# Performance work log

Hardware: AMD Instinct MI355X
Metric: run time of the kernel (lower is better)

## Reference

```python
import jax, jax.numpy as jnp
import numpy as np

NUM_CLASSES = 1000
FEAT_DIM = 512
BATCH = 16384


def setup_inputs() -> dict:
    key = jax.random.key(0)
    k1, k2, k3 = jax.random.split(key, 3)
    x = jax.random.normal(k1, (BATCH, FEAT_DIM), dtype=jnp.float32)
    labels = jax.random.randint(k2, (BATCH,), 0, NUM_CLASSES, dtype=jnp.int64)
    centers = jax.random.normal(k3, (NUM_CLASSES, FEAT_DIM), dtype=jnp.float32)
    margin = jnp.ones((1,), dtype=jnp.float32)
    return {"x": x, "labels": labels, "centers": centers, "margin": margin}


def reference(x, labels, centers, margin):
    # squared euclidean distances: [B, C]
    distmat = (
        jnp.sum(x * x, axis=1, keepdims=True)
        + jnp.sum(centers * centers, axis=1)[None, :]
        - 2.0 * (x @ centers.T)
    )
    B, C = distmat.shape
    onehot = labels[:, None] == jnp.arange(C, dtype=labels.dtype)[None, :]  # [B, C]
    # distance to the true-class center
    dist = jnp.sum(jnp.where(onehot, distmat, 0.0), axis=1)  # [B]
    # min distance over all other classes (mask true class with +inf)
    dist_min = jnp.min(jnp.where(onehot, jnp.inf, distmat), axis=1)  # [B]
    m = margin[0]
    loss = jnp.sum(jnp.maximum(m + dist - dist_min, 0.0)) / B
    return loss
```

## Files before the change

kernel.cpp:

```cpp
#include <hip/hip_runtime.h>
#include <hip/hip_bf16.h>

#define BATCH 16384
#define NCLS  1000
#define NPAD  1024
#define FDIM  512

#define CBLK_STRIDE 266240
#define TAIL_OFF    262144

typedef __bf16 bf16x4 __attribute__((ext_vector_type(4)));
typedef __bf16 bf16x8 __attribute__((ext_vector_type(8)));
typedef float  f32x16 __attribute__((ext_vector_type(16)));

#define GLOBAL_AS __attribute__((address_space(1)))
#define LDS_AS    __attribute__((address_space(3)))

#define VMCNT(n) asm volatile("s_waitcnt vmcnt(" #n ")" ::: "memory")
#define LGKM0()  asm volatile("s_waitcnt lgkmcnt(0)" ::: "memory")
#define BAR()    do { LGKM0(); __builtin_amdgcn_s_barrier(); \
                      __builtin_amdgcn_sched_barrier(0); } while (0)

__global__ __launch_bounds__(64) void prep_centers(
    const float* __restrict__ centers, char* __restrict__ cbt,
    float* __restrict__ out)
{
    const int c = blockIdx.x, t = threadIdx.x;
    const int cblk = c >> 8, cl = c & 255;
    char* base = cbt + (size_t)cblk * CBLK_STRIDE;
    if (c == 0 && t == 0) out[0] = 0.f;

    float4 f0 = make_float4(0.f, 0.f, 0.f, 0.f);
    float4 f1 = make_float4(0.f, 0.f, 0.f, 0.f);
    if (c < NCLS) {
        f0 = *(const float4*)(centers + (size_t)c * FDIM + t * 8);
        f1 = *(const float4*)(centers + (size_t)c * FDIM + t * 8 + 4);
    }
    bf16x8 b;
    b[0] = (__bf16)f0.x; b[1] = (__bf16)f0.y; b[2] = (__bf16)f0.z; b[3] = (__bf16)f0.w;
    b[4] = (__bf16)f1.x; b[5] = (__bf16)f1.y; b[6] = (__bf16)f1.z; b[7] = (__bf16)f1.w;
    *(bf16x8*)(base + (t >> 2) * 16384 + (t & 3) * 4096 + cl * 16) = b;

    float ssum = f0.x*f0.x + f0.y*f0.y + f0.z*f0.z + f0.w*f0.w
               + f1.x*f1.x + f1.y*f1.y + f1.z*f1.z + f1.w*f1.w;
    #pragma unroll
    for (int o = 32; o > 0; o >>= 1) ssum += __shfl_down(ssum, o);
    if (t == 0) {
        const float hf = (c < NCLS) ? (-0.5f * ssum) : -1e30f;
        const __bf16 h = (__bf16)hf;
        const __bf16 l = (c < NCLS) ? (__bf16)(hf - (float)h) : (__bf16)0.f;
        bf16x8 tl;
        #pragma unroll
        for (int e = 0; e < 8; ++e) tl[e] = (__bf16)0.f;
        tl[0] = h; tl[1] = l;
        *(bf16x8*)(base + TAIL_OFF + cl * 16) = tl;
    }
}

struct B2 { float4 a, b; };

__global__ __launch_bounds__(512, 4) void trip_main(
    const float* __restrict__ x, const int* __restrict__ labels,
    const char* __restrict__ cbt, float* __restrict__ mxp,
    float* __restrict__ dap)
{
    extern __shared__ char lds[];
    const int t    = threadIdx.x;
    const int lane = t & 63;
    const int w    = t >> 6;
    const int wM   = w >> 1, wN = w & 1;
    const int l31  = lane & 31, hi = lane >> 5;
    const int bid  = blockIdx.x;
    const int cblk = bid >> 7;
    const int bblk = bid & 127;
    const int class0 = cblk * 256;
    const int row0   = bblk * 128;
    const char* cbB  = cbt + (size_t)cblk * CBLK_STRIDE;

    auto stageA = [&](int ko, int ai) {
        const char* src = cbB + ko * 16384 + t * 16;
        char* dst = lds + ai * 16384 + t * 16;
        __builtin_amdgcn_global_load_lds((const GLOBAL_AS void*)src,
                                         (LDS_AS void*)dst, 16, 0, 0);
        __builtin_amdgcn_global_load_lds((const GLOBAL_AS void*)(src + 8192),
                                         (LDS_AS void*)(dst + 8192), 16, 0, 0);
    };
    auto loadB = [&](int ko, B2& br) {
        const float* src = x + (size_t)(row0 + w * 16 + (lane >> 3)) * FDIM
                         + ko * 32 + (lane & 7) * 4;
        br.a = *(const float4*)(src);
        br.b = *(const float4*)(src + 8 * FDIM);
    };
    auto cv4 = [](float4 f) {
        bf16x4 v;
        v[0] = (__bf16)f.x; v[1] = (__bf16)f.y;
        v[2] = (__bf16)f.z; v[3] = (__bf16)f.w;
        return v;
    };
    auto writeB = [&](const B2& br, int bi) {
        char* dst = lds + 32768 + bi * 8192 + ((lane & 7) >> 1) * 2048
                  + (w * 16 + (lane >> 3)) * 16 + (lane & 1) * 8;
        *(bf16x4*)(dst      ) = cv4(br.a);
        *(bf16x4*)(dst + 128) = cv4(br.b);
    };

    f32x16 acc[2][2];
    #pragma unroll
    for (int mi = 0; mi < 2; ++mi)
        #pragma unroll
        for (int ni = 0; ni < 2; ++ni)
            #pragma unroll
            for (int r = 0; r < 16; ++r) acc[mi][ni][r] = 0.f;

    auto compute = [&](int buf) {
        const char* A = lds + buf * 16384;
        const char* B = lds + 32768 + buf * 8192;
        #pragma unroll
        for (int ks = 0; ks < 2; ++ks) {
            const int chunk = ks * 2 + hi;
            bf16x8 a0 = *(const bf16x8*)(A + chunk * 4096 + (wM * 64 +  0 + l31) * 16);
            bf16x8 a1 = *(const bf16x8*)(A + chunk * 4096 + (wM * 64 + 32 + l31) * 16);
            bf16x8 b0 = *(const bf16x8*)(B + chunk * 2048 + (wN * 64 +  0 + l31) * 16);
            bf16x8 b1 = *(const bf16x8*)(B + chunk * 2048 + (wN * 64 + 32 + l31) * 16);
            acc[0][0] = __builtin_amdgcn_mfma_f32_32x32x16_bf16(a0, b0, acc[0][0], 0, 0, 0);
            acc[0][1] = __builtin_amdgcn_mfma_f32_32x32x16_bf16(a0, b1, acc[0][1], 0, 0, 0);
            acc[1][0] = __builtin_amdgcn_mfma_f32_32x32x16_bf16(a1, b0, acc[1][0], 0, 0, 0);
            acc[1][1] = __builtin_amdgcn_mfma_f32_32x32x16_bf16(a1, b1, acc[1][1], 0, 0, 0);
        }
    };

    const int lab0 = labels[row0 + wN * 64 + l31];
    const int lab1 = labels[row0 + wN * 64 + 32 + l31];
    if (t < 256) {
        const char* src = cbB + TAIL_OFF + t * 16;
        char* dst = lds + 49152 + t * 16;
        __builtin_amdgcn_global_load_lds((const GLOBAL_AS void*)src,
                                         (LDS_AS void*)dst, 16, 0, 0);
    }
    B2 brA, brB;
    stageA(0, 0); loadB(0, brA);
    __builtin_amdgcn_sched_barrier(0);
    loadB(1, brB);
    VMCNT(2);
    writeB(brA, 0);
    BAR();

    #pragma unroll
    for (int tt = 0; tt < 16; ++tt) {
        const int cur = tt & 1, oth = cur ^ 1;
        if (tt < 15) stageA(tt + 1, oth);
        if (tt <= 13) {
            if (tt & 1) loadB(tt + 2, brB);
            else        loadB(tt + 2, brA);
        }
        if (tt <= 13)      VMCNT(2);
        else if (tt == 14) VMCNT(0);
        if (tt <= 14) {
            if (tt & 1) writeB(brA, oth);
            else        writeB(brB, oth);
        }
        compute(cur);
        BAR();
    }

    {
        const char* T = lds + 49152;
        bf16x8 bt;
        #pragma unroll
        for (int e = 0; e < 8; ++e) bt[e] = (__bf16)0.f;
        if (hi == 0) { bt[0] = (__bf16)1.0f; bt[1] = (__bf16)1.0f; }
        #pragma unroll
        for (int mi = 0; mi < 2; ++mi) {
            bf16x8 a = *(const bf16x8*)(T + (wM * 64 + mi * 32 + l31) * 16);
            #pragma unroll
            for (int ni = 0; ni < 2; ++ni)
                acc[mi][ni] = __builtin_amdgcn_mfma_f32_32x32x16_bf16(
                    a, bt, acc[mi][ni], 0, 0, 0);
        }
    }

    const int labBase = class0 + wM * 64 + hi * 4;
    const int labA0 = lab0 - labBase;
    const int labA1 = lab1 - labBase;
    float MX0 = -3e38f, MX1 = -3e38f, DA0 = -3e38f, DA1 = -3e38f;
    #pragma unroll
    for (int mi = 0; mi < 2; ++mi) {
        #pragma unroll
        for (int r = 0; r < 16; ++r) {
            const int pat = mi * 32 + (r & 3) + 8 * (r >> 2);
            {
                const float a = acc[mi][0][r];
                const bool is = (labA0 == pat);
                MX0 = fmaxf(MX0, is ? -3e38f : a);
                DA0 = is ? a : DA0;
            }
            {
                const float a = acc[mi][1][r];
                const bool is = (labA1 == pat);
                MX1 = fmaxf(MX1, is ? -3e38f : a);
                DA1 = is ? a : DA1;
            }
        }
    }
    MX0 = fmaxf(MX0, __shfl_xor(MX0, 32));
    DA0 = fmaxf(DA0, __shfl_xor(DA0, 32));
    MX1 = fmaxf(MX1, __shfl_xor(MX1, 32));
    DA1 = fmaxf(DA1, __shfl_xor(DA1, 32));

    float* scm = (float*)lds;
    float* scd = scm + 512;
    __syncthreads();
    if (hi == 0) {
        const int r0 = wN * 64 + l31;
        scm[wM * 128 + r0]      = MX0;  scd[wM * 128 + r0]      = DA0;
        scm[wM * 128 + r0 + 32] = MX1;  scd[wM * 128 + r0 + 32] = DA1;
    }
    __syncthreads();
    if (t < 128) {
        const float mx = fmaxf(fmaxf(scm[t], scm[128 + t]),
                               fmaxf(scm[256 + t], scm[384 + t]));
        const float da = fmaxf(fmaxf(scd[t], scd[128 + t]),
                               fmaxf(scd[256 + t], scd[384 + t]));
        mxp[cblk * BATCH + row0 + t] = mx;
        dap[cblk * BATCH + row0 + t] = da;
    }
}

__global__ __launch_bounds__(256) void combine(
    const float* __restrict__ mxp, const float* __restrict__ dap,
    const float* __restrict__ margin, float* __restrict__ out)
{
    const int t = threadIdx.x;
    const int row = blockIdx.x * 256 + t;
    float mx = fmaxf(fmaxf(mxp[row], mxp[BATCH + row]),
                     fmaxf(mxp[2 * BATCH + row], mxp[3 * BATCH + row]));
    float da = fmaxf(fmaxf(dap[row], dap[BATCH + row]),
                     fmaxf(dap[2 * BATCH + row], dap[3 * BATCH + row]));
    float loss = fmaxf(margin[0] - 2.f * da + 2.f * mx, 0.f);
    __shared__ float red[4];
    #pragma unroll
    for (int o = 32; o > 0; o >>= 1) loss += __shfl_down(loss, o);
    if ((t & 63) == 0) red[t >> 6] = loss;
    __syncthreads();
    if (t == 0)
        atomicAdd(out, (red[0] + red[1] + red[2] + red[3]) * (1.0f / BATCH));
}

extern "C" void kernel_launch(void* const* d_in, const int* in_sizes, int n_in,
                              void* d_out, int out_size, void* d_ws, size_t ws_size,
                              hipStream_t stream)
{
    const float* x       = (const float*)d_in[0];
    const int*   labels  = (const int*)d_in[1];
    const float* centers = (const float*)d_in[2];
    const float* margin  = (const float*)d_in[3];
    float* out = (float*)d_out;

    char* ws = (char*)d_ws;
    char*  cbt  = ws;
    float* mxp  = (float*)(ws + 1064960);
    float* dap  = (float*)(ws + 1327104);

    (void)hipFuncSetAttribute((const void*)trip_main,
                              hipFuncAttributeMaxDynamicSharedMemorySize, 53248);

    prep_centers<<<NPAD, 64, 0, stream>>>(centers, cbt, out);
    trip_main<<<512, 512, 53248, stream>>>(x, labels, cbt, mxp, dap);
    combine<<<64, 256, 0, stream>>>(mxp, dap, margin, out);
}
```

Before: 33.18 us.

## Widen class tile to 512 per block and split K-steps with barrier-scheduled MFMA phases

Each block now covers 512 classes instead of 256, so the grid shrinks to 256 blocks with 90 KB of LDS, and x is read and converted half as often. The main loop splits each K tile into two phases separated by barriers, uses s_setprio around the MFMA bursts, and interleaves global-to-LDS staging with compute. The prep kernel packs four classes per block, and combine reduces only two partials. In exchange occupancy drops to one block per CU, and 256 blocks may underfill the GPU.

```diff
diff --git a/kernel.cpp b/kernel.cpp
--- a/kernel.cpp
+++ b/kernel.cpp
@@ -3,13 +3,11 @@
 
 #define BATCH 16384
 #define NCLS  1000
-#define NPAD  1024
 #define FDIM  512
 
-#define CBLK_STRIDE 266240
-#define TAIL_OFF    262144
-
-typedef __bf16 bf16x4 __attribute__((ext_vector_type(4)));
+#define CBLK_STRIDE 532480
+#define TAIL_OFF    524288
+
 typedef __bf16 bf16x8 __attribute__((ext_vector_type(8)));
 typedef float  f32x16 __attribute__((ext_vector_type(16)));
 
@@ -18,34 +16,37 @@
 
 #define VMCNT(n) asm volatile("s_waitcnt vmcnt(" #n ")" ::: "memory")
 #define LGKM0()  asm volatile("s_waitcnt lgkmcnt(0)" ::: "memory")
-#define BAR()    do { LGKM0(); __builtin_amdgcn_s_barrier(); \
-                      __builtin_amdgcn_sched_barrier(0); } while (0)
-
-__global__ __launch_bounds__(64) void prep_centers(
+#define SBAR()   __builtin_amdgcn_s_barrier()
+#define SCHED0() __builtin_amdgcn_sched_barrier(0)
+
+__global__ __launch_bounds__(256) void prep(
     const float* __restrict__ centers, char* __restrict__ cbt,
     float* __restrict__ out)
 {
-    const int c = blockIdx.x, t = threadIdx.x;
-    const int cblk = c >> 8, cl = c & 255;
+    const int bid = blockIdx.x, t = threadIdx.x;
+    if (bid == 0 && t == 0) out[0] = 0.f;
+
+    const int lane = t & 63;
+    const int c = bid * 4 + (t >> 6);
+    const int cblk = c >> 9, cl = c & 511;
     char* base = cbt + (size_t)cblk * CBLK_STRIDE;
-    if (c == 0 && t == 0) out[0] = 0.f;
 
     float4 f0 = make_float4(0.f, 0.f, 0.f, 0.f);
     float4 f1 = make_float4(0.f, 0.f, 0.f, 0.f);
     if (c < NCLS) {
-        f0 = *(const float4*)(centers + (size_t)c * FDIM + t * 8);
-        f1 = *(const float4*)(centers + (size_t)c * FDIM + t * 8 + 4);
+        f0 = *(const float4*)(centers + (size_t)c * FDIM + lane * 8);
+        f1 = *(const float4*)(centers + (size_t)c * FDIM + lane * 8 + 4);
     }
     bf16x8 b;
     b[0] = (__bf16)f0.x; b[1] = (__bf16)f0.y; b[2] = (__bf16)f0.z; b[3] = (__bf16)f0.w;
     b[4] = (__bf16)f1.x; b[5] = (__bf16)f1.y; b[6] = (__bf16)f1.z; b[7] = (__bf16)f1.w;
-    *(bf16x8*)(base + (t >> 2) * 16384 + (t & 3) * 4096 + cl * 16) = b;
+    *(bf16x8*)(base + (lane >> 2) * 32768 + (lane & 3) * 8192 + cl * 16) = b;
 
     float ssum = f0.x*f0.x + f0.y*f0.y + f0.z*f0.z + f0.w*f0.w
                + f1.x*f1.x + f1.y*f1.y + f1.z*f1.z + f1.w*f1.w;
     #pragma unroll
     for (int o = 32; o > 0; o >>= 1) ssum += __shfl_down(ssum, o);
-    if (t == 0) {
+    if (lane == 0) {
         const float hf = (c < NCLS) ? (-0.5f * ssum) : -1e30f;
         const __bf16 h = (__bf16)hf;
         const __bf16 l = (c < NCLS) ? (__bf16)(hf - (float)h) : (__bf16)0.f;
@@ -57,9 +58,9 @@
     }
 }
 
-struct B2 { float4 a, b; };
-
-__global__ __launch_bounds__(512, 4) void trip_main(
+struct Bst { float4 f0, f1; };
+
+__global__ __launch_bounds__(512, 1) void trip_main(
     const float* __restrict__ x, const int* __restrict__ labels,
     const char* __restrict__ cbt, float* __restrict__ mxp,
     float* __restrict__ dap)
@@ -73,105 +74,134 @@
     const int bid  = blockIdx.x;
     const int cblk = bid >> 7;
     const int bblk = bid & 127;
-    const int class0 = cblk * 256;
+    const int class0 = cblk * 512;
     const int row0   = bblk * 128;
     const char* cbB  = cbt + (size_t)cblk * CBLK_STRIDE;
 
-    auto stageA = [&](int ko, int ai) {
-        const char* src = cbB + ko * 16384 + t * 16;
-        char* dst = lds + ai * 16384 + t * 16;
-        __builtin_amdgcn_global_load_lds((const GLOBAL_AS void*)src,
-                                         (LDS_AS void*)dst, 16, 0, 0);
-        __builtin_amdgcn_global_load_lds((const GLOBAL_AS void*)(src + 8192),
-                                         (LDS_AS void*)(dst + 8192), 16, 0, 0);
+    const int rB = t & 127, cB = t >> 7;
+    const float* xb = x + (size_t)(row0 + rB) * FDIM + cB * 8;
+
+    auto stageA = [&](int T1, int buf) {
+        const char* src = cbB + T1 * 32768 + t * 16;
+        char* dst = lds + buf * 32768 + t * 16;
+        #pragma unroll
+        for (int j = 0; j < 4; ++j)
+            __builtin_amdgcn_global_load_lds(
+                (const GLOBAL_AS void*)(src + j * 8192),
+                (LDS_AS void*)(dst + j * 8192), 16, 0, 0);
     };
-    auto loadB = [&](int ko, B2& br) {
-        const float* src = x + (size_t)(row0 + w * 16 + (lane >> 3)) * FDIM
-                         + ko * 32 + (lane & 7) * 4;
-        br.a = *(const float4*)(src);
-        br.b = *(const float4*)(src + 8 * FDIM);
+    auto loadB = [&](int T2, Bst& s) {
+        const float* src = xb + T2 * 32;
+        s.f0 = *(const float4*)(src);
+        s.f1 = *(const float4*)(src + 4);
     };
-    auto cv4 = [](float4 f) {
-        bf16x4 v;
-        v[0] = (__bf16)f.x; v[1] = (__bf16)f.y;
-        v[2] = (__bf16)f.z; v[3] = (__bf16)f.w;
-        return v;
+    auto writeB = [&](const Bst& s, int buf) {
+        bf16x8 v;
+        v[0] = (__bf16)s.f0.x; v[1] = (__bf16)s.f0.y;
+        v[2] = (__bf16)s.f0.z; v[3] = (__bf16)s.f0.w;
+        v[4] = (__bf16)s.f1.x; v[5] = (__bf16)s.f1.y;
+        v[6] = (__bf16)s.f1.z; v[7] = (__bf16)s.f1.w;
+        *(bf16x8*)(lds + 65536 + buf * 8192 + cB * 2048 + rB * 16) = v;
     };
-    auto writeB = [&](const B2& br, int bi) {
-        char* dst = lds + 32768 + bi * 8192 + ((lane & 7) >> 1) * 2048
-                  + (w * 16 + (lane >> 3)) * 16 + (lane & 1) * 8;
-        *(bf16x4*)(dst      ) = cv4(br.a);
-        *(bf16x4*)(dst + 128) = cv4(br.b);
-    };
-
-    f32x16 acc[2][2];
-    #pragma unroll
-    for (int mi = 0; mi < 2; ++mi)
+
+    f32x16 acc[4][2];
+    #pragma unroll
+    for (int mi = 0; mi < 4; ++mi)
         #pragma unroll
         for (int ni = 0; ni < 2; ++ni)
             #pragma unroll
             for (int r = 0; r < 16; ++r) acc[mi][ni][r] = 0.f;
 
-    auto compute = [&](int buf) {
-        const char* A = lds + buf * 16384;
-        const char* B = lds + 32768 + buf * 8192;
-        #pragma unroll
-        for (int ks = 0; ks < 2; ++ks) {
-            const int chunk = ks * 2 + hi;
-            bf16x8 a0 = *(const bf16x8*)(A + chunk * 4096 + (wM * 64 +  0 + l31) * 16);
-            bf16x8 a1 = *(const bf16x8*)(A + chunk * 4096 + (wM * 64 + 32 + l31) * 16);
-            bf16x8 b0 = *(const bf16x8*)(B + chunk * 2048 + (wN * 64 +  0 + l31) * 16);
-            bf16x8 b1 = *(const bf16x8*)(B + chunk * 2048 + (wN * 64 + 32 + l31) * 16);
+    const int lab0 = labels[row0 + wN * 64 + l31];
+    const int lab1 = labels[row0 + wN * 64 + 32 + l31];
+    SCHED0();
+    {
+        const char* src = cbB + TAIL_OFF + t * 16;
+        char* dst = lds + 81920 + t * 16;
+        __builtin_amdgcn_global_load_lds((const GLOBAL_AS void*)src,
+                                         (LDS_AS void*)dst, 16, 0, 0);
+    }
+    SCHED0();
+    Bst bX, bY;
+    stageA(0, 0);
+    loadB(0, bX);
+    SCHED0();
+    loadB(1, bY);
+    VMCNT(2);
+    writeB(bX, 0);
+    LGKM0(); SBAR(); SCHED0();
+
+    #pragma unroll
+    for (int T = 0; T < 16; ++T) {
+        const int cur = T & 1, oth = cur ^ 1;
+        const char* A  = lds + cur * 32768;
+        const char* Bb = lds + 65536 + cur * 8192;
+        {
+            const int chunk = hi;
+            bf16x8 a0 = *(const bf16x8*)(A + chunk * 8192 + (wM * 128 +  0 + l31) * 16);
+            bf16x8 a1 = *(const bf16x8*)(A + chunk * 8192 + (wM * 128 + 32 + l31) * 16);
+            bf16x8 a2 = *(const bf16x8*)(A + chunk * 8192 + (wM * 128 + 64 + l31) * 16);
+            bf16x8 a3 = *(const bf16x8*)(A + chunk * 8192 + (wM * 128 + 96 + l31) * 16);
+            bf16x8 b0 = *(const bf16x8*)(Bb + chunk * 2048 + (wN * 64 +  0 + l31) * 16);
+            bf16x8 b1 = *(const bf16x8*)(Bb + chunk * 2048 + (wN * 64 + 32 + l31) * 16);
+            if (T < 15) stageA(T + 1, oth);
+            if (T < 14) {
+                if (T & 1) loadB(T + 2, bY);
+                else       loadB(T + 2, bX);
+            }
+            SBAR(); LGKM0(); SCHED0();
+            __builtin_amdgcn_s_setprio(1);
             acc[0][0] = __builtin_amdgcn_mfma_f32_32x32x16_bf16(a0, b0, acc[0][0], 0, 0, 0);
             acc[0][1] = __builtin_amdgcn_mfma_f32_32x32x16_bf16(a0, b1, acc[0][1], 0, 0, 0);
             acc[1][0] = __builtin_amdgcn_mfma_f32_32x32x16_bf16(a1, b0, acc[1][0], 0, 0, 0);
             acc[1][1] = __builtin_amdgcn_mfma_f32_32x32x16_bf16(a1, b1, acc[1][1], 0, 0, 0);
-        }
-    };
-
-    const int lab0 = labels[row0 + wN * 64 + l31];
-    const int lab1 = labels[row0 + wN * 64 + 32 + l31];
-    if (t < 256) {
-        const char* src = cbB + TAIL_OFF + t * 16;
-        char* dst = lds + 49152 + t * 16;
-        __builtin_amdgcn_global_load_lds((const GLOBAL_AS void*)src,
-                                         (LDS_AS void*)dst, 16, 0, 0);
-    }
-    B2 brA, brB;
-    stageA(0, 0); loadB(0, brA);
-    __builtin_amdgcn_sched_barrier(0);
-    loadB(1, brB);
-    VMCNT(2);
-    writeB(brA, 0);
-    BAR();
-
-    #pragma unroll
-    for (int tt = 0; tt < 16; ++tt) {
-        const int cur = tt & 1, oth = cur ^ 1;
-        if (tt < 15) stageA(tt + 1, oth);
-        if (tt <= 13) {
-            if (tt & 1) loadB(tt + 2, brB);
-            else        loadB(tt + 2, brA);
-        }
-        if (tt <= 13)      VMCNT(2);
-        else if (tt == 14) VMCNT(0);
-        if (tt <= 14) {
-            if (tt & 1) writeB(brA, oth);
-            else        writeB(brB, oth);
-        }
-        compute(cur);
-        BAR();
+            acc[2][0] = __builtin_amdgcn_mfma_f32_32x32x16_bf16(a2, b0, acc[2][0], 0, 0, 0);
+            acc[2][1] = __builtin_amdgcn_mfma_f32_32x32x16_bf16(a2, b1, acc[2][1], 0, 0, 0);
+            acc[3][0] = __builtin_amdgcn_mfma_f32_32x32x16_bf16(a3, b0, acc[3][0], 0, 0, 0);
+            acc[3][1] = __builtin_amdgcn_mfma_f32_32x32x16_bf16(a3, b1, acc[3][1], 0, 0, 0);
+            __builtin_amdgcn_s_setprio(0);
+            SBAR(); SCHED0();
+        }
+        {
+            const int chunk = 2 + hi;
+            bf16x8 a0 = *(const bf16x8*)(A + chunk * 8192 + (wM * 128 +  0 + l31) * 16);
+            bf16x8 a1 = *(const bf16x8*)(A + chunk * 8192 + (wM * 128 + 32 + l31) * 16);
+            bf16x8 a2 = *(const bf16x8*)(A + chunk * 8192 + (wM * 128 + 64 + l31) * 16);
+            bf16x8 a3 = *(const bf16x8*)(A + chunk * 8192 + (wM * 128 + 96 + l31) * 16);
+            bf16x8 b0 = *(const bf16x8*)(Bb + chunk * 2048 + (wN * 64 +  0 + l31) * 16);
+            bf16x8 b1 = *(const bf16x8*)(Bb + chunk * 2048 + (wN * 64 + 32 + l31) * 16);
+            if (T <= 13)      VMCNT(6);
+            else if (T == 14) VMCNT(4);
+            if (T <= 14) {
+                if (T & 1) writeB(bX, oth);
+                else       writeB(bY, oth);
+            }
+            if (T <= 13)      VMCNT(2);
+            else if (T == 14) VMCNT(0);
+            SBAR(); LGKM0(); SCHED0();
+            __builtin_amdgcn_s_setprio(1);
+            acc[0][0] = __builtin_amdgcn_mfma_f32_32x32x16_bf16(a0, b0, acc[0][0], 0, 0, 0);
+            acc[0][1] = __builtin_amdgcn_mfma_f32_32x32x16_bf16(a0, b1, acc[0][1], 0, 0, 0);
+            acc[1][0] = __builtin_amdgcn_mfma_f32_32x32x16_bf16(a1, b0, acc[1][0], 0, 0, 0);
+            acc[1][1] = __builtin_amdgcn_mfma_f32_32x32x16_bf16(a1, b1, acc[1][1], 0, 0, 0);
+            acc[2][0] = __builtin_amdgcn_mfma_f32_32x32x16_bf16(a2, b0, acc[2][0], 0, 0, 0);
+            acc[2][1] = __builtin_amdgcn_mfma_f32_32x32x16_bf16(a2, b1, acc[2][1], 0, 0, 0);
+            acc[3][0] = __builtin_amdgcn_mfma_f32_32x32x16_bf16(a3, b0, acc[3][0], 0, 0, 0);
+            acc[3][1] = __builtin_amdgcn_mfma_f32_32x32x16_bf16(a3, b1, acc[3][1], 0, 0, 0);
+            __builtin_amdgcn_s_setprio(0);
+            SBAR(); SCHED0();
+        }
     }
 
     {
-        const char* T = lds + 49152;
+        const char* Tl = lds + 81920;
         bf16x8 bt;
         #pragma unroll
         for (int e = 0; e < 8; ++e) bt[e] = (__bf16)0.f;
         if (hi == 0) { bt[0] = (__bf16)1.0f; bt[1] = (__bf16)1.0f; }
         #pragma unroll
-        for (int mi = 0; mi < 2; ++mi) {
-            bf16x8 a = *(const bf16x8*)(T + (wM * 64 + mi * 32 + l31) * 16);
+        for (int mi = 0; mi < 4; ++mi) {
+            bf16x8 a = *(const bf16x8*)(Tl + (wM * 128 + mi * 32 + l31) * 16);
             #pragma unroll
             for (int ni = 0; ni < 2; ++ni)
                 acc[mi][ni] = __builtin_amdgcn_mfma_f32_32x32x16_bf16(
@@ -179,12 +209,12 @@
         }
     }
 
-    const int labBase = class0 + wM * 64 + hi * 4;
+    const int labBase = class0 + wM * 128 + hi * 4;
     const int labA0 = lab0 - labBase;
     const int labA1 = lab1 - labBase;
     float MX0 = -3e38f, MX1 = -3e38f, DA0 = -3e38f, DA1 = -3e38f;
     #pragma unroll
-    for (int mi = 0; mi < 2; ++mi) {
+    for (int mi = 0; mi < 4; ++mi) {
         #pragma unroll
         for (int r = 0; r < 16; ++r) {
             const int pat = mi * 32 + (r & 3) + 8 * (r >> 2);
@@ -232,10 +262,8 @@
 {
     const int t = threadIdx.x;
     const int row = blockIdx.x * 256 + t;
-    float mx = fmaxf(fmaxf(mxp[row], mxp[BATCH + row]),
-                     fmaxf(mxp[2 * BATCH + row], mxp[3 * BATCH + row]));
-    float da = fmaxf(fmaxf(dap[row], dap[BATCH + row]),
-                     fmaxf(dap[2 * BATCH + row], dap[3 * BATCH + row]));
+    const float mx = fmaxf(mxp[row], mxp[BATCH + row]);
+    const float da = fmaxf(dap[row], dap[BATCH + row]);
     float loss = fmaxf(margin[0] - 2.f * da + 2.f * mx, 0.f);
     __shared__ float red[4];
     #pragma unroll
@@ -259,12 +287,12 @@
     char* ws = (char*)d_ws;
     char*  cbt  = ws;
     float* mxp  = (float*)(ws + 1064960);
-    float* dap  = (float*)(ws + 1327104);
+    float* dap  = (float*)(ws + 1196032);
 
     (void)hipFuncSetAttribute((const void*)trip_main,
-                              hipFuncAttributeMaxDynamicSharedMemorySize, 53248);
-
-    prep_centers<<<NPAD, 64, 0, stream>>>(centers, cbt, out);
-    trip_main<<<512, 512, 53248, stream>>>(x, labels, cbt, mxp, dap);
+                              hipFuncAttributeMaxDynamicSharedMemorySize, 90112);
+
+    prep<<<256, 256, 0, stream>>>(centers, cbt, out);
+    trip_main<<<256, 512, 90112, stream>>>(x, labels, cbt, mxp, dap);
     combine<<<64, 256, 0, stream>>>(mxp, dap, margin, out);
 }
```

After: 39.45 us. +18.9%, slower.
